# Performance work log

Hardware: AMD Instinct MI355X
Metric: run time of the kernel (lower is better)

The kernel has to match this reference:

```python
import jax, jax.numpy as jnp
import numpy as np

N, E, DIM, HEADS, EDGE_DIM = 50000, 800000, 128, 4, 1
C = DIM // HEADS  # per-head channels
EPS = 1e-5


def graph_ln(h, w, b):
    # PyG LayerNorm, mode='graph', batch=None: normalize over ALL nodes+features
    mu = h.mean()
    hc = h - mu
    std = jnp.sqrt(jnp.mean(hc * hc))
    return hc / (std + EPS) * w + b


def setup_inputs() -> dict:
    key = jax.random.key(0)
    ks = jax.random.split(key, 16)
    s = 1.0 / np.sqrt(DIM)
    return {
        "x": jax.random.normal(ks[0], (N, DIM), jnp.float32),
        "edge_index": jax.random.randint(ks[1], (2, E), 0, N, jnp.int32),
        "edge_weight": jax.random.uniform(ks[2], (E,), jnp.float32),
        "edge_attr": jax.random.normal(ks[3], (E, EDGE_DIM), jnp.float32),
        # GCNConv params
        "W_gcn": jax.random.normal(ks[4], (DIM, DIM), jnp.float32) * s,
        "b_gcn": jnp.zeros((DIM,), jnp.float32),
        # GATv2Conv params (share_weights=True -> single lin)
        "W_l": jax.random.normal(ks[5], (DIM, DIM), jnp.float32) * s,
        "b_l": jnp.zeros((DIM,), jnp.float32),
        "W_edge": jax.random.normal(ks[6], (EDGE_DIM, DIM), jnp.float32),
        "att": jax.random.normal(ks[7], (HEADS, C), jnp.float32) * (1.0 / np.sqrt(C)),
        "b_gat": jnp.zeros((DIM,), jnp.float32),
        # norms
        "gcn_nw": jnp.ones((DIM,), jnp.float32), "gcn_nb": jnp.zeros((DIM,), jnp.float32),
        "gat_nw": jnp.ones((DIM,), jnp.float32), "gat_nb": jnp.zeros((DIM,), jnp.float32),
        "out_nw": jnp.ones((DIM,), jnp.float32), "out_nb": jnp.zeros((DIM,), jnp.float32),
        "alpha": jnp.ones((2,), jnp.float32),
    }


def reference(x, edge_index, edge_weight, edge_attr, W_gcn, b_gcn, W_l, b_l,
              W_edge, att, b_gat, gcn_nw, gcn_nb, gat_nw, gat_nb, out_nw, out_nb, alpha):
    src, dst = edge_index[0], edge_index[1]

    # ---- GCN branch (normalize=True, add_self_loops=False) ----
    deg = jax.ops.segment_sum(edge_weight, dst, num_segments=N)
    dis = jnp.where(deg > 0, jax.lax.rsqrt(jnp.maximum(deg, 1e-30)), 0.0)
    norm = dis[src] * edge_weight * dis[dst]  # [E]
    xw = x @ W_gcn  # [N, DIM]
    h = jax.ops.segment_sum(norm[:, None] * xw[src], dst, num_segments=N) + b_gcn
    gcn_out = x + jax.nn.gelu(graph_ln(h, gcn_nw, gcn_nb), approximate=False)

    # ---- GATv2 branch (share_weights=True, edge_dim=1) ----
    xl = (x @ W_l + b_l).reshape(N, HEADS, C)
    e = (edge_attr @ W_edge).reshape(E, HEADS, C)
    z = jax.nn.leaky_relu(xl[dst] + xl[src] + e, negative_slope=0.2)  # [E,H,C]
    logits = jnp.einsum('ehc,hc->eh', z, att)  # [E,H]
    m = jax.ops.segment_max(logits, dst, num_segments=N)  # [N,H]
    a = jnp.exp(logits - m[dst])
    denom = jax.ops.segment_sum(a, dst, num_segments=N)
    a = a / (denom[dst] + 1e-16)  # softmax over incoming edges per dst, per head
    msg = xl[src] * a[:, :, None]  # [E,H,C]
    g = jax.ops.segment_sum(msg, dst, num_segments=N).reshape(N, DIM) + b_gat
    gat_out = x + jax.nn.gelu(graph_ln(g, gat_nw, gat_nb), approximate=False)

    # ---- fuse ----
    w = jax.nn.softmax(alpha)
    fused = w[0] * gcn_out + w[1] * gat_out
    return jax.nn.gelu(graph_ln(fused, out_nw, out_nb), approximate=False)
```

## Files before the change

kernel.cpp:

```cpp
#include <hip/hip_runtime.h>
#include <math.h>

#define DIM 128
#define HEADS 4
#define EPS 1e-5f
#define NBLK 1024

__device__ __forceinline__ float us2f(unsigned short u) {
  union { unsigned int i; float f; } c; c.i = ((unsigned int)u) << 16; return c.f;
}
__device__ __forceinline__ unsigned short f2us(float f) {
  union { float ff; unsigned int i; } c; c.ff = f;
  return (unsigned short)((c.i + 0x7FFFu + ((c.i >> 16) & 1u)) >> 16);
}
__device__ __forceinline__ float ldf(const void* p, size_t i, int fl32) {
  return fl32 ? ((const float*)p)[i] : us2f(((const unsigned short*)p)[i]);
}
__device__ __forceinline__ float gelu_exact(float v) {
  return 0.5f * v * (1.0f + erff(v * 0.7071067811865475f));
}

__global__ void __launch_bounds__(256)
k_detect(const unsigned short* __restrict__ x, long n, int* __restrict__ dflag) {
  long lim = n < 8192 ? n : 8192;
  int bad = 0;
  for (long i = threadIdx.x; i < lim; i += 256) {
    float v = us2f(x[i]);
    float a = fabsf(v);
    if (!(a == 0.0f || (a > 1e-30f && a < 1e3f))) bad++;
  }
  __shared__ int sb[256];
  sb[threadIdx.x] = bad;
  __syncthreads();
  for (int off = 128; off > 0; off >>= 1) {
    if ((int)threadIdx.x < off) sb[threadIdx.x] += sb[threadIdx.x + off];
    __syncthreads();
  }
  if (threadIdx.x == 0) dflag[0] = (sb[0] > 32) ? 1 : 0;
}

__global__ void k_deg_cnt(const int* __restrict__ dst, const void* __restrict__ ew,
                          float* __restrict__ deg, int* __restrict__ cnt, int E,
                          const int* __restrict__ df) {
  const int fl32 = *df;
  int e = blockIdx.x * blockDim.x + threadIdx.x;
  if (e < E) {
    int d = dst[e];
    float w = ldf(ew, e, fl32);
    if (isfinite(w)) atomicAdd(&deg[d], w);
    atomicAdd(&cnt[d], 1);
  }
}

__global__ void k_dis(float* __restrict__ deg, int N) {
  int i = blockIdx.x * blockDim.x + threadIdx.x;
  if (i < N) {
    float d = deg[i];
    deg[i] = (d > 0.0f) ? rsqrtf(fmaxf(d, 1e-30f)) : 0.0f;
  }
}

__global__ void __launch_bounds__(256)
k_scan(const int* __restrict__ cnt, int* __restrict__ off, int N, int E) {
  __shared__ int part[256];
  int t = threadIdx.x;
  int chunk = (N + 255) / 256;
  int lo = t * chunk;
  int hi = lo + chunk; if (hi > N) hi = N;
  int s = 0;
  for (int i = lo; i < hi; ++i) s += cnt[i];
  part[t] = s;
  __syncthreads();
  if (t == 0) {
    int run = 0;
    for (int j = 0; j < 256; ++j) { int tmp = part[j]; part[j] = run; run += tmp; }
  }
  __syncthreads();
  int run = part[t];
  for (int i = lo; i < hi; ++i) { off[i] = run; run += cnt[i]; }
  if (t == 0) off[N] = E;
}

__global__ void k_scatter(const int* __restrict__ src, const int* __restrict__ dst,
                          const void* __restrict__ ew, const void* __restrict__ ea,
                          const float* __restrict__ dis, const int* __restrict__ off,
                          int* __restrict__ cursor, int* __restrict__ csr_src,
                          float* __restrict__ csr_nm, float* __restrict__ csr_ea,
                          int E, const int* __restrict__ df) {
  const int fl32 = *df;
  int e = blockIdx.x * blockDim.x + threadIdx.x;
  if (e >= E) return;
  int d = dst[e], s = src[e];
  int pos = off[d] + atomicAdd(&cursor[d], 1);
  csr_src[pos] = s;
  float nm = dis[s] * ldf(ew, e, fl32) * dis[d];
  if (!isfinite(nm)) nm = 0.0f;
  csr_nm[pos] = nm;
  float eav = ldf(ea, e, fl32);
  if (!isfinite(eav)) eav = 0.0f;
  csr_ea[pos] = eav;
}

__global__ void __launch_bounds__(128)
k_gemm_dual(const void* __restrict__ x, const void* __restrict__ Wg,
            const void* __restrict__ Wl, const void* __restrict__ bl,
            unsigned short* __restrict__ xw, unsigned short* __restrict__ xl, int N,
            const int* __restrict__ df) {
  const int fl32 = *df;
  const int R = 8;
  __shared__ float xs[R][DIM];
  int c = threadIdx.x;
  int r0 = blockIdx.x * R;
  for (int r = 0; r < R; ++r) {
    int row = r0 + r;
    xs[r][c] = (row < N) ? ldf(x, (size_t)row * DIM + c, fl32) : 0.0f;
  }
  __syncthreads();
  float accg[R], accl[R];
  float blc = ldf(bl, c, fl32);
  #pragma unroll
  for (int r = 0; r < R; ++r) { accg[r] = 0.0f; accl[r] = blc; }
  for (int k = 0; k < DIM; ++k) {
    float wg = ldf(Wg, k * DIM + c, fl32);
    float wl = ldf(Wl, k * DIM + c, fl32);
    #pragma unroll
    for (int r = 0; r < R; ++r) {
      accg[r] = fmaf(xs[r][k], wg, accg[r]);
      accl[r] = fmaf(xs[r][k], wl, accl[r]);
    }
  }
  for (int r = 0; r < R; ++r) {
    int row = r0 + r;
    if (row < N) {
      float ag = accg[r], al = accl[r];
      if (!isfinite(ag)) ag = 0.0f;
      if (!isfinite(al)) al = 0.0f;
      xw[(size_t)row * DIM + c] = f2us(ag);
      xl[(size_t)row * DIM + c] = f2us(al);
    }
  }
}

__global__ void __launch_bounds__(256)
k_mega(const int* __restrict__ off, const int* __restrict__ csr_src,
       const float* __restrict__ csr_nm, const float* __restrict__ csr_ea,
       const unsigned short* __restrict__ xw, const unsigned short* __restrict__ xl,
       const void* __restrict__ Wed, const void* __restrict__ att,
       const void* __restrict__ bgcn, const void* __restrict__ bgat,
       float* __restrict__ h, float* __restrict__ g,
       double* __restrict__ pA, double* __restrict__ pB, int N,
       const int* __restrict__ df) {
  const int fl32 = *df;
  int wid = threadIdx.x >> 6;
  int lane = threadIdx.x & 63;
  int node = blockIdx.x * 4 + wid;
  int c0 = lane * 2;
  float wd0 = ldf(Wed, c0, fl32), wd1 = ldf(Wed, c0 + 1, fl32);
  float at0 = ldf(att, c0, fl32), at1 = ldf(att, c0 + 1, fl32);
  double sA = 0.0, sA2 = 0.0, sB = 0.0, sB2 = 0.0;
  if (node < N) {
    int beg = off[node], end = off[node + 1];
    float xd0 = us2f(xl[(size_t)node * DIM + c0]);
    float xd1 = us2f(xl[(size_t)node * DIM + c0 + 1]);
    float mx = -INFINITY, den = 0.f;
    float ga0 = 0.f, ga1 = 0.f, hc0 = 0.f, hc1 = 0.f;
    float eaP = 0.f, nmP = 0.f;
    ushort2 vP = make_ushort2(0, 0), uP = make_ushort2(0, 0);
    if (beg < end) {
      int s0 = csr_src[beg];
      eaP = csr_ea[beg];
      nmP = csr_nm[beg];
      vP = *(const ushort2*)(xl + (size_t)s0 * DIM + c0);
      uP = *(const ushort2*)(xw + (size_t)s0 * DIM + c0);
    }
    for (int i = beg; i < end; ++i) {
      float eav = eaP, nm = nmP;
      ushort2 v = vP, u = uP;
      int inext = i + 1;
      if (inext < end) {
        int sN = csr_src[inext];
        eaP = csr_ea[inext];
        nmP = csr_nm[inext];
        vP = *(const ushort2*)(xl + (size_t)sN * DIM + c0);
        uP = *(const ushort2*)(xw + (size_t)sN * DIM + c0);
      }
      float vx = us2f(v.x), vy = us2f(v.y);
      float z0 = xd0 + vx + eav * wd0; z0 = (z0 > 0.f) ? z0 : 0.2f * z0;
      float z1 = xd1 + vy + eav * wd1; z1 = (z1 > 0.f) ? z1 : 0.2f * z1;
      float dot = z0 * at0 + z1 * at1;
      dot += __shfl_xor(dot, 1);
      dot += __shfl_xor(dot, 2);
      dot += __shfl_xor(dot, 4);
      dot += __shfl_xor(dot, 8);
      if (!isfinite(dot)) dot = 0.0f;
      float nmx = fmaxf(mx, dot);
      float corr = __expf(mx - nmx);
      float w = __expf(dot - nmx);
      mx = nmx;
      den = fmaf(den, corr, w);
      ga0 = fmaf(ga0, corr, w * vx);
      ga1 = fmaf(ga1, corr, w * vy);
      hc0 = fmaf(nm, us2f(u.x), hc0);
      hc1 = fmaf(nm, us2f(u.y), hc1);
    }
    float inv = (end > beg) ? 1.0f / (den + 1e-16f) : 0.0f;
    ga0 *= inv; ga1 *= inv;
    if (!isfinite(ga0)) ga0 = 0.0f;
    if (!isfinite(ga1)) ga1 = 0.0f;
    if (!isfinite(hc0)) hc0 = 0.0f;
    if (!isfinite(hc1)) hc1 = 0.0f;
    *(float2*)(h + (size_t)node * DIM + c0) = make_float2(hc0, hc1);
    *(float2*)(g + (size_t)node * DIM + c0) = make_float2(ga0, ga1);
    float hA0 = hc0 + ldf(bgcn, c0, fl32), hA1 = hc1 + ldf(bgcn, c0 + 1, fl32);
    float gB0 = ga0 + ldf(bgat, c0, fl32), gB1 = ga1 + ldf(bgat, c0 + 1, fl32);
    sA  = (double)hA0 + (double)hA1;
    sA2 = (double)hA0 * hA0 + (double)hA1 * hA1;
    sB  = (double)gB0 + (double)gB1;
    sB2 = (double)gB0 * gB0 + (double)gB1 * gB1;
  }
  __shared__ double l1[256], l2[256], l3[256], l4[256];
  l1[threadIdx.x] = sA; l2[threadIdx.x] = sA2; l3[threadIdx.x] = sB; l4[threadIdx.x] = sB2;
  __syncthreads();
  for (int o = 128; o > 0; o >>= 1) {
    if ((int)threadIdx.x < o) {
      l1[threadIdx.x] += l1[threadIdx.x + o];
      l2[threadIdx.x] += l2[threadIdx.x + o];
      l3[threadIdx.x] += l3[threadIdx.x + o];
      l4[threadIdx.x] += l4[threadIdx.x + o];
    }
    __syncthreads();
  }
  if (threadIdx.x == 0) {
    pA[2 * blockIdx.x] = l1[0]; pA[2 * blockIdx.x + 1] = l2[0];
    pB[2 * blockIdx.x] = l3[0]; pB[2 * blockIdx.x + 1] = l4[0];
  }
}

__device__ __forceinline__ void ln_params(double S, double S2, double M, float* mu_out, float* sc_out) {
  double mu = S / M;
  double v = S2 / M - mu * mu;
  if (!(v > 0.0)) v = 0.0;
  float fmu = (float)mu;
  float sc = 1.0f / ((float)sqrt(v) + EPS);
  if (!isfinite(fmu)) fmu = 0.0f;
  if (!isfinite(sc)) sc = 0.0f;
  *mu_out = fmu; *sc_out = sc;
}

__global__ void __launch_bounds__(256)
k_fin12(const double* __restrict__ pA, const double* __restrict__ pB, int nblk,
        const void* __restrict__ alpha, float* __restrict__ params, double M,
        const int* __restrict__ df) {
  const int fl32 = *df;
  __shared__ double l1[256], l2[256], l3[256], l4[256];
  double a = 0, b = 0, c = 0, d = 0;
  for (int j = threadIdx.x; j < nblk; j += 256) {
    a += pA[2 * j]; b += pA[2 * j + 1];
    c += pB[2 * j]; d += pB[2 * j + 1];
  }
  l1[threadIdx.x] = a; l2[threadIdx.x] = b; l3[threadIdx.x] = c; l4[threadIdx.x] = d;
  __syncthreads();
  for (int off = 128; off > 0; off >>= 1) {
    if ((int)threadIdx.x < off) {
      l1[threadIdx.x] += l1[threadIdx.x + off];
      l2[threadIdx.x] += l2[threadIdx.x + off];
      l3[threadIdx.x] += l3[threadIdx.x + off];
      l4[threadIdx.x] += l4[threadIdx.x + off];
    }
    __syncthreads();
  }
  if (threadIdx.x == 0) {
    ln_params(l1[0], l2[0], M, &params[0], &params[1]);
    ln_params(l3[0], l4[0], M, &params[2], &params[3]);
    float a0 = ldf(alpha, 0, fl32), a1 = ldf(alpha, 1, fl32);
    if (!isfinite(a0)) a0 = 0.0f;
    if (!isfinite(a1)) a1 = 0.0f;
    float mx = fmaxf(a0, a1);
    float e0 = expf(a0 - mx), e1 = expf(a1 - mx);
    float inv = 1.0f / (e0 + e1);
    params[4] = e0 * inv;
    params[5] = e1 * inv;
  }
}

__global__ void __launch_bounds__(256)
k_fin3(const double* __restrict__ pC, float* __restrict__ params, double M) {
  __shared__ double l1[256], l2[256];
  double a = 0, b = 0;
  for (int j = threadIdx.x; j < NBLK; j += 256) { a += pC[2 * j]; b += pC[2 * j + 1]; }
  l1[threadIdx.x] = a; l2[threadIdx.x] = b;
  __syncthreads();
  for (int off = 128; off > 0; off >>= 1) {
    if ((int)threadIdx.x < off) {
      l1[threadIdx.x] += l1[threadIdx.x + off];
      l2[threadIdx.x] += l2[threadIdx.x + off];
    }
    __syncthreads();
  }
  if (threadIdx.x == 0) ln_params(l1[0], l2[0], M, &params[6], &params[7]);
}

__global__ void __launch_bounds__(256)
k_fuse(const void* __restrict__ x, float* h, const float* __restrict__ g,
       const void* __restrict__ b_gcn, const void* __restrict__ b_gat,
       const void* __restrict__ gcn_nw, const void* __restrict__ gcn_nb,
       const void* __restrict__ gat_nw, const void* __restrict__ gat_nb,
       const float* __restrict__ params, double* __restrict__ pC, long n,
       const int* __restrict__ df) {
  const int fl32 = *df;
  float mu1 = params[0], sc1 = params[1], mu2 = params[2], sc2 = params[3];
  float w0 = params[4], w1 = params[5];
  double s = 0.0, s2 = 0.0;
  long stride = (long)gridDim.x * blockDim.x;
  for (long i = (long)blockIdx.x * blockDim.x + threadIdx.x; i < n; i += stride) {
    size_t c = (size_t)(i & (DIM - 1));
    float xv = ldf(x, i, fl32);
    float hv = h[i] + ldf(b_gcn, c, fl32);
    float gv = g[i] + ldf(b_gat, c, fl32);
    float go = xv + gelu_exact((hv - mu1) * sc1 * ldf(gcn_nw, c, fl32) + ldf(gcn_nb, c, fl32));
    float ao = xv + gelu_exact((gv - mu2) * sc2 * ldf(gat_nw, c, fl32) + ldf(gat_nb, c, fl32));
    float f = w0 * go + w1 * ao;
    if (!isfinite(f)) f = 0.0f;
    h[i] = f;
    s += f; s2 += (double)f * f;
  }
  __shared__ double ls[256], ls2[256];
  ls[threadIdx.x] = s; ls2[threadIdx.x] = s2;
  __syncthreads();
  for (int off = 128; off > 0; off >>= 1) {
    if ((int)threadIdx.x < off) {
      ls[threadIdx.x] += ls[threadIdx.x + off];
      ls2[threadIdx.x] += ls2[threadIdx.x + off];
    }
    __syncthreads();
  }
  if (threadIdx.x == 0) { pC[2 * blockIdx.x] = ls[0]; pC[2 * blockIdx.x + 1] = ls2[0]; }
}

__global__ void k_final(const float* __restrict__ fused, const void* __restrict__ nw,
                        const void* __restrict__ nb, const float* __restrict__ params,
                        void* __restrict__ out, long n, const int* __restrict__ df) {
  const int fl32 = *df;
  long i = (long)blockIdx.x * blockDim.x + threadIdx.x;
  if (i >= n) return;
  size_t c = (size_t)(i & (DIM - 1));
  float mu = params[6], sc = params[7];
  float r = gelu_exact((fused[i] - mu) * sc * ldf(nw, c, fl32) + ldf(nb, c, fl32));
  if (!isfinite(r)) r = 0.0f;
  if (fl32) ((float*)out)[i] = r;
  else      ((unsigned short*)out)[i] = f2us(r);
}

extern "C" void kernel_launch(void* const* d_in, const int* in_sizes, int n_in,
                              void* d_out, int out_size, void* d_ws, size_t ws_size,
                              hipStream_t stream) {
  const void* x    = d_in[0];
  const int*  ei   = (const int*)d_in[1];
  const void* ew   = d_in[2];
  const void* ea   = d_in[3];
  const void* Wg   = d_in[4];
  const void* bgcn = d_in[5];
  const void* Wl   = d_in[6];
  const void* bl   = d_in[7];
  const void* Wed  = d_in[8];
  const void* att  = d_in[9];
  const void* bgat = d_in[10];
  const void* gcn_nw = d_in[11];
  const void* gcn_nb = d_in[12];
  const void* gat_nw = d_in[13];
  const void* gat_nb = d_in[14];
  const void* out_nw = d_in[15];
  const void* out_nb = d_in[16];
  const void* alpha  = d_in[17];

  const int N = in_sizes[0] / DIM;
  const int E = in_sizes[2];
  const int* src  = ei;
  const int* dstp = ei + E;
  const size_t ND = (size_t)N * DIM;
  const int nAgg = (N + 3) / 4;

  char* ws = (char*)d_ws;
  size_t o = 0;
  auto alloc = [&](size_t bytes) { size_t r = o; o += (bytes + 255) & ~(size_t)255; return r; };
  size_t o_deg    = alloc((size_t)N * 4);
  size_t o_cnt    = alloc((size_t)N * 4);
  size_t o_cursor = alloc((size_t)N * 4);
  size_t zero_end = o;
  size_t o_off    = alloc((size_t)(N + 1) * 4);
  size_t o_h      = alloc(ND * 4);
  size_t o_g      = alloc(ND * 4);
  size_t o_xw     = alloc(ND * 2);
  size_t o_xl     = alloc(ND * 2);
  size_t o_csrc   = alloc((size_t)E * 4);
  size_t o_cnm    = alloc((size_t)E * 4);
  size_t o_cea    = alloc((size_t)E * 4);
  size_t o_par    = alloc(8 * 4);
  size_t o_pA     = alloc((size_t)nAgg * 2 * 8);
  size_t o_pB     = alloc((size_t)nAgg * 2 * 8);
  size_t o_pC     = alloc((size_t)NBLK * 2 * 8);
  size_t o_flag   = alloc(4);
  (void)ws_size; (void)n_in; (void)out_size;

  float* deg     = (float*)(ws + o_deg);
  int*   cnt     = (int*)(ws + o_cnt);
  int*   cursor  = (int*)(ws + o_cursor);
  int*   off     = (int*)(ws + o_off);
  float* h       = (float*)(ws + o_h);
  float* g       = (float*)(ws + o_g);
  unsigned short* xw = (unsigned short*)(ws + o_xw);
  unsigned short* xl = (unsigned short*)(ws + o_xl);
  int*   csr_src = (int*)(ws + o_csrc);
  float* csr_nm  = (float*)(ws + o_cnm);
  float* csr_ea  = (float*)(ws + o_cea);
  float* params  = (float*)(ws + o_par);
  double* pA     = (double*)(ws + o_pA);
  double* pB     = (double*)(ws + o_pB);
  double* pC     = (double*)(ws + o_pC);
  int* dflag     = (int*)(ws + o_flag);

  hipMemsetAsync(ws, 0, zero_end, stream);
  k_detect<<<1, 256, 0, stream>>>((const unsigned short*)x, (long)ND, dflag);

  int ebk = (E + 255) / 256;
  k_deg_cnt<<<ebk, 256, 0, stream>>>(dstp, ew, deg, cnt, E, dflag);
  k_dis<<<(N + 255) / 256, 256, 0, stream>>>(deg, N);
  k_scan<<<1, 256, 0, stream>>>(cnt, off, N, E);
  k_scatter<<<ebk, 256, 0, stream>>>(src, dstp, ew, ea, deg, off, cursor,
                                     csr_src, csr_nm, csr_ea, E, dflag);

  k_gemm_dual<<<(N + 7) / 8, 128, 0, stream>>>(x, Wg, Wl, bl, xw, xl, N, dflag);

  k_mega<<<nAgg, 256, 0, stream>>>(off, csr_src, csr_nm, csr_ea, xw, xl,
                                   Wed, att, bgcn, bgat, h, g, pA, pB, N, dflag);

  k_fin12<<<1, 256, 0, stream>>>(pA, pB, nAgg, alpha, params, (double)ND, dflag);
  k_fuse<<<NBLK, 256, 0, stream>>>(x, h, g, bgcn, bgat, gcn_nw, gcn_nb, gat_nw, gat_nb,
                                   params, pC, (long)ND, dflag);
  k_fin3<<<1, 256, 0, stream>>>(pC, params, (double)ND);
  k_final<<<(int)((ND + 255) / 256), 256, 0, stream>>>(h, out_nw, out_nb, params,
                                                       d_out, (long)ND, dflag);
}
```

Measured before the change: 572.4 us.

## Use bf16 MFMA for dual GEMM, interleave xl/xw and pack CSR into int4

Replaces the scalar FMA dual GEMM with bf16 MFMA 16x16x32 using pre-swizzled weight fragments. The GEMM writes xl and xw interleaved per row, so the aggregation kernel fetches both with a single 8-byte gather per edge. CSR src/norm/edge_attr are packed into one int4 per edge, and the per-edge atomic rank is computed in the degree pass, which removes the cursor atomics from the scatter. The online softmax update is also rewritten to need one exp instead of two. The extra prepW kernel adds a launch, and the fp32 fallback path is a slow naive loop.

```diff
diff --git a/kernel.cpp b/kernel.cpp
--- a/kernel.cpp
+++ b/kernel.cpp
@@ -6,6 +6,10 @@
 #define EPS 1e-5f
 #define NBLK 1024
 
+typedef short frag_ab __attribute__((ext_vector_type(8)));
+typedef float f32x4 __attribute__((ext_vector_type(4)));
+typedef unsigned short us8 __attribute__((ext_vector_type(8)));
+
 __device__ __forceinline__ float us2f(unsigned short u) {
   union { unsigned int i; float f; } c; c.i = ((unsigned int)u) << 16; return c.f;
 }
@@ -19,6 +23,8 @@
 __device__ __forceinline__ float gelu_exact(float v) {
   return 0.5f * v * (1.0f + erff(v * 0.7071067811865475f));
 }
+
+__device__ __forceinline__ int packed_pos(int c) { return ((c & ~1) << 1) | (c & 1); }
 
 __global__ void __launch_bounds__(256)
 k_detect(const unsigned short* __restrict__ x, long n, int* __restrict__ dflag) {
@@ -40,15 +46,15 @@
 }
 
 __global__ void k_deg_cnt(const int* __restrict__ dst, const void* __restrict__ ew,
-                          float* __restrict__ deg, int* __restrict__ cnt, int E,
-                          const int* __restrict__ df) {
+                          float* __restrict__ deg, int* __restrict__ cnt,
+                          int* __restrict__ rank, int E, const int* __restrict__ df) {
   const int fl32 = *df;
   int e = blockIdx.x * blockDim.x + threadIdx.x;
   if (e < E) {
     int d = dst[e];
+    rank[e] = atomicAdd(&cnt[d], 1);
     float w = ldf(ew, e, fl32);
     if (isfinite(w)) atomicAdd(&deg[d], w);
-    atomicAdd(&cnt[d], 1);
   }
 }
 
@@ -84,67 +90,117 @@
 __global__ void k_scatter(const int* __restrict__ src, const int* __restrict__ dst,
                           const void* __restrict__ ew, const void* __restrict__ ea,
                           const float* __restrict__ dis, const int* __restrict__ off,
-                          int* __restrict__ cursor, int* __restrict__ csr_src,
-                          float* __restrict__ csr_nm, float* __restrict__ csr_ea,
+                          const int* __restrict__ rank, int4* __restrict__ csr,
                           int E, const int* __restrict__ df) {
   const int fl32 = *df;
   int e = blockIdx.x * blockDim.x + threadIdx.x;
   if (e >= E) return;
   int d = dst[e], s = src[e];
-  int pos = off[d] + atomicAdd(&cursor[d], 1);
-  csr_src[pos] = s;
+  int pos = off[d] + rank[e];
   float nm = dis[s] * ldf(ew, e, fl32) * dis[d];
   if (!isfinite(nm)) nm = 0.0f;
-  csr_nm[pos] = nm;
   float eav = ldf(ea, e, fl32);
   if (!isfinite(eav)) eav = 0.0f;
-  csr_ea[pos] = eav;
-}
-
-__global__ void __launch_bounds__(128)
-k_gemm_dual(const void* __restrict__ x, const void* __restrict__ Wg,
-            const void* __restrict__ Wl, const void* __restrict__ bl,
-            unsigned short* __restrict__ xw, unsigned short* __restrict__ xl, int N,
-            const int* __restrict__ df) {
-  const int fl32 = *df;
-  const int R = 8;
-  __shared__ float xs[R][DIM];
-  int c = threadIdx.x;
-  int r0 = blockIdx.x * R;
-  for (int r = 0; r < R; ++r) {
-    int row = r0 + r;
-    xs[r][c] = (row < N) ? ldf(x, (size_t)row * DIM + c, fl32) : 0.0f;
-  }
-  __syncthreads();
-  float accg[R], accl[R];
-  float blc = ldf(bl, c, fl32);
+  csr[pos] = make_int4(s, __float_as_int(nm), __float_as_int(eav), 0);
+}
+
+__global__ void __launch_bounds__(256)
+k_prepW(const unsigned short* __restrict__ Wg, const unsigned short* __restrict__ Wl,
+        unsigned short* __restrict__ Wtg, unsigned short* __restrict__ Wtl) {
+  int idx = blockIdx.x * 256 + threadIdx.x;
+  if (idx >= 2048) return;
+  int kc = idx >> 9, rem = idx & 511, nt = rem >> 6, lane = rem & 63;
+  int quad = lane >> 4, n = lane & 15;
   #pragma unroll
-  for (int r = 0; r < R; ++r) { accg[r] = 0.0f; accl[r] = blc; }
-  for (int k = 0; k < DIM; ++k) {
-    float wg = ldf(Wg, k * DIM + c, fl32);
-    float wl = ldf(Wl, k * DIM + c, fl32);
+  for (int j = 0; j < 8; ++j) {
+    int srcIdx = (kc * 32 + quad * 8 + j) * DIM + nt * 16 + n;
+    Wtg[idx * 8 + j] = Wg[srcIdx];
+    Wtl[idx * 8 + j] = Wl[srcIdx];
+  }
+}
+
+__global__ void __launch_bounds__(256)
+k_gemm(const void* __restrict__ x, const void* __restrict__ Wg, const void* __restrict__ Wl,
+       const void* __restrict__ bl, const unsigned short* __restrict__ Wtg,
+       const unsigned short* __restrict__ Wtl, unsigned short* __restrict__ packed,
+       int N, const int* __restrict__ df) {
+  const int fl32 = *df;
+  __shared__ unsigned short tiles[4][16][256];
+  int wid = threadIdx.x >> 6, lane = threadIdx.x & 63;
+  int quad = lane >> 4, m = lane & 15;
+  int row0 = blockIdx.x * 64 + wid * 16;
+  if (!fl32) {
+    const unsigned short* xb = (const unsigned short*)x;
+    int rowm = row0 + m;
+    frag_ab a[4];
     #pragma unroll
-    for (int r = 0; r < R; ++r) {
-      accg[r] = fmaf(xs[r][k], wg, accg[r]);
-      accl[r] = fmaf(xs[r][k], wl, accl[r]);
-    }
-  }
-  for (int r = 0; r < R; ++r) {
-    int row = r0 + r;
-    if (row < N) {
-      float ag = accg[r], al = accl[r];
-      if (!isfinite(ag)) ag = 0.0f;
-      if (!isfinite(al)) al = 0.0f;
-      xw[(size_t)row * DIM + c] = f2us(ag);
-      xl[(size_t)row * DIM + c] = f2us(al);
-    }
-  }
-}
-
-__global__ void __launch_bounds__(256)
-k_mega(const int* __restrict__ off, const int* __restrict__ csr_src,
-       const float* __restrict__ csr_nm, const float* __restrict__ csr_ea,
-       const unsigned short* __restrict__ xw, const unsigned short* __restrict__ xl,
+    for (int kc = 0; kc < 4; ++kc) {
+      if (rowm < N) a[kc] = *(const frag_ab*)(xb + (size_t)rowm * DIM + kc * 32 + quad * 8);
+      else { frag_ab z; for (int j = 0; j < 8; ++j) z[j] = 0; a[kc] = z; }
+    }
+    f32x4 accG[8], accL[8];
+    #pragma unroll
+    for (int nt = 0; nt < 8; ++nt)
+      for (int r = 0; r < 4; ++r) { accG[nt][r] = 0.f; accL[nt][r] = 0.f; }
+    #pragma unroll
+    for (int nt = 0; nt < 8; ++nt) {
+      #pragma unroll
+      for (int kc = 0; kc < 4; ++kc) {
+        frag_ab bg = *(const frag_ab*)(Wtg + ((size_t)(kc * 8 + nt) * 64 + lane) * 8);
+        frag_ab bf = *(const frag_ab*)(Wtl + ((size_t)(kc * 8 + nt) * 64 + lane) * 8);
+        accG[nt] = __builtin_amdgcn_mfma_f32_16x16x32_bf16(a[kc], bg, accG[nt], 0, 0, 0);
+        accL[nt] = __builtin_amdgcn_mfma_f32_16x16x32_bf16(a[kc], bf, accL[nt], 0, 0, 0);
+      }
+    }
+    #pragma unroll
+    for (int nt = 0; nt < 8; ++nt) {
+      int c = nt * 16 + m;
+      float blc = us2f(((const unsigned short*)bl)[c]);
+      int pos = packed_pos(c);
+      #pragma unroll
+      for (int r = 0; r < 4; ++r) {
+        int row = quad * 4 + r;
+        float vG = accG[nt][r];
+        float vL = accL[nt][r] + blc;
+        if (!isfinite(vG)) vG = 0.f;
+        if (!isfinite(vL)) vL = 0.f;
+        tiles[wid][row][pos] = f2us(vL);
+        tiles[wid][row][pos + 2] = f2us(vG);
+      }
+    }
+    __syncthreads();
+    #pragma unroll
+    for (int t = 0; t < 8; ++t) {
+      int flat = t * 512 + lane * 8;
+      int r = flat >> 8, cp = flat & 255;
+      int grow = row0 + r;
+      if (grow < N)
+        *(us8*)(packed + (size_t)grow * 256 + cp) = *(const us8*)&tiles[wid][r][cp];
+    }
+  } else {
+    int c = threadIdx.x & 127;
+    float blc = ldf(bl, c, 1);
+    for (int rr = (threadIdx.x >> 7); rr < 64; rr += 2) {
+      int row = blockIdx.x * 64 + rr;
+      if (row >= N) continue;
+      float ag = 0.f, al = blc;
+      for (int k = 0; k < DIM; ++k) {
+        float xv = ldf(x, (size_t)row * DIM + k, 1);
+        ag = fmaf(xv, ldf(Wg, k * DIM + c, 1), ag);
+        al = fmaf(xv, ldf(Wl, k * DIM + c, 1), al);
+      }
+      if (!isfinite(ag)) ag = 0.f;
+      if (!isfinite(al)) al = 0.f;
+      int pos = packed_pos(c);
+      packed[(size_t)row * 256 + pos] = f2us(al);
+      packed[(size_t)row * 256 + pos + 2] = f2us(ag);
+    }
+  }
+}
+
+__global__ void __launch_bounds__(256)
+k_mega(const int* __restrict__ off, const int4* __restrict__ csr,
+       const unsigned short* __restrict__ packed,
        const void* __restrict__ Wed, const void* __restrict__ att,
        const void* __restrict__ bgcn, const void* __restrict__ bgat,
        float* __restrict__ h, float* __restrict__ g,
@@ -160,30 +216,23 @@
   double sA = 0.0, sA2 = 0.0, sB = 0.0, sB2 = 0.0;
   if (node < N) {
     int beg = off[node], end = off[node + 1];
-    float xd0 = us2f(xl[(size_t)node * DIM + c0]);
-    float xd1 = us2f(xl[(size_t)node * DIM + c0 + 1]);
+    ushort4 xd = *(const ushort4*)(packed + (size_t)node * 256 + lane * 4);
+    float xd0 = us2f(xd.x), xd1 = us2f(xd.y);
     float mx = -INFINITY, den = 0.f;
     float ga0 = 0.f, ga1 = 0.f, hc0 = 0.f, hc1 = 0.f;
-    float eaP = 0.f, nmP = 0.f;
-    ushort2 vP = make_ushort2(0, 0), uP = make_ushort2(0, 0);
+    int4 cP = make_int4(0, 0, 0, 0);
+    ushort4 vP = make_ushort4(0, 0, 0, 0);
     if (beg < end) {
-      int s0 = csr_src[beg];
-      eaP = csr_ea[beg];
-      nmP = csr_nm[beg];
-      vP = *(const ushort2*)(xl + (size_t)s0 * DIM + c0);
-      uP = *(const ushort2*)(xw + (size_t)s0 * DIM + c0);
+      cP = csr[beg];
+      vP = *(const ushort4*)(packed + (size_t)cP.x * 256 + lane * 4);
     }
     for (int i = beg; i < end; ++i) {
-      float eav = eaP, nm = nmP;
-      ushort2 v = vP, u = uP;
-      int inext = i + 1;
-      if (inext < end) {
-        int sN = csr_src[inext];
-        eaP = csr_ea[inext];
-        nmP = csr_nm[inext];
-        vP = *(const ushort2*)(xl + (size_t)sN * DIM + c0);
-        uP = *(const ushort2*)(xw + (size_t)sN * DIM + c0);
+      int4 ce = cP; ushort4 v = vP;
+      if (i + 1 < end) {
+        cP = csr[i + 1];
+        vP = *(const ushort4*)(packed + (size_t)cP.x * 256 + lane * 4);
       }
+      float nm = __int_as_float(ce.y), eav = __int_as_float(ce.z);
       float vx = us2f(v.x), vy = us2f(v.y);
       float z0 = xd0 + vx + eav * wd0; z0 = (z0 > 0.f) ? z0 : 0.2f * z0;
       float z1 = xd1 + vy + eav * wd1; z1 = (z1 > 0.f) ? z1 : 0.2f * z1;
@@ -192,16 +241,16 @@
       dot += __shfl_xor(dot, 2);
       dot += __shfl_xor(dot, 4);
       dot += __shfl_xor(dot, 8);
-      if (!isfinite(dot)) dot = 0.0f;
-      float nmx = fmaxf(mx, dot);
-      float corr = __expf(mx - nmx);
-      float w = __expf(dot - nmx);
-      mx = nmx;
+      float e = __expf(-fabsf(dot - mx));
+      bool up = dot > mx;
+      float corr = up ? e : 1.0f;
+      float w = up ? 1.0f : e;
+      mx = up ? dot : mx;
       den = fmaf(den, corr, w);
       ga0 = fmaf(ga0, corr, w * vx);
       ga1 = fmaf(ga1, corr, w * vy);
-      hc0 = fmaf(nm, us2f(u.x), hc0);
-      hc1 = fmaf(nm, us2f(u.y), hc1);
+      hc0 = fmaf(nm, us2f(v.z), hc0);
+      hc1 = fmaf(nm, us2f(v.w), hc1);
     }
     float inv = (end > beg) ? 1.0f / (den + 1e-16f) : 0.0f;
     ga0 *= inv; ga1 *= inv;
@@ -385,16 +434,14 @@
   auto alloc = [&](size_t bytes) { size_t r = o; o += (bytes + 255) & ~(size_t)255; return r; };
   size_t o_deg    = alloc((size_t)N * 4);
   size_t o_cnt    = alloc((size_t)N * 4);
-  size_t o_cursor = alloc((size_t)N * 4);
   size_t zero_end = o;
   size_t o_off    = alloc((size_t)(N + 1) * 4);
   size_t o_h      = alloc(ND * 4);
   size_t o_g      = alloc(ND * 4);
-  size_t o_xw     = alloc(ND * 2);
-  size_t o_xl     = alloc(ND * 2);
-  size_t o_csrc   = alloc((size_t)E * 4);
-  size_t o_cnm    = alloc((size_t)E * 4);
-  size_t o_cea    = alloc((size_t)E * 4);
+  size_t o_packed = alloc(ND * 4);
+  size_t o_csr    = alloc((size_t)E * 16);
+  size_t o_wtg    = alloc(2048 * 8 * 2);
+  size_t o_wtl    = alloc(2048 * 8 * 2);
   size_t o_par    = alloc(8 * 4);
   size_t o_pA     = alloc((size_t)nAgg * 2 * 8);
   size_t o_pB     = alloc((size_t)nAgg * 2 * 8);
@@ -404,15 +451,14 @@
 
   float* deg     = (float*)(ws + o_deg);
   int*   cnt     = (int*)(ws + o_cnt);
-  int*   cursor  = (int*)(ws + o_cursor);
   int*   off     = (int*)(ws + o_off);
   float* h       = (float*)(ws + o_h);
+  int*   rank    = (int*)(ws + o_h);
   float* g       = (float*)(ws + o_g);
-  unsigned short* xw = (unsigned short*)(ws + o_xw);
-  unsigned short* xl = (unsigned short*)(ws + o_xl);
-  int*   csr_src = (int*)(ws + o_csrc);
-  float* csr_nm  = (float*)(ws + o_cnm);
-  float* csr_ea  = (float*)(ws + o_cea);
+  unsigned short* packed = (unsigned short*)(ws + o_packed);
+  int4*  csr     = (int4*)(ws + o_csr);
+  unsigned short* Wtg = (unsigned short*)(ws + o_wtg);
+  unsigned short* Wtl = (unsigned short*)(ws + o_wtl);
   float* params  = (float*)(ws + o_par);
   double* pA     = (double*)(ws + o_pA);
   double* pB     = (double*)(ws + o_pB);
@@ -423,16 +469,16 @@
   k_detect<<<1, 256, 0, stream>>>((const unsigned short*)x, (long)ND, dflag);
 
   int ebk = (E + 255) / 256;
-  k_deg_cnt<<<ebk, 256, 0, stream>>>(dstp, ew, deg, cnt, E, dflag);
+  k_deg_cnt<<<ebk, 256, 0, stream>>>(dstp, ew, deg, cnt, rank, E, dflag);
   k_dis<<<(N + 255) / 256, 256, 0, stream>>>(deg, N);
   k_scan<<<1, 256, 0, stream>>>(cnt, off, N, E);
-  k_scatter<<<ebk, 256, 0, stream>>>(src, dstp, ew, ea, deg, off, cursor,
-                                     csr_src, csr_nm, csr_ea, E, dflag);
-
-  k_gemm_dual<<<(N + 7) / 8, 128, 0, stream>>>(x, Wg, Wl, bl, xw, xl, N, dflag);
-
-  k_mega<<<nAgg, 256, 0, stream>>>(off, csr_src, csr_nm, csr_ea, xw, xl,
-                                   Wed, att, bgcn, bgat, h, g, pA, pB, N, dflag);
+  k_scatter<<<ebk, 256, 0, stream>>>(src, dstp, ew, ea, deg, off, rank, csr, E, dflag);
+
+  k_prepW<<<8, 256, 0, stream>>>((const unsigned short*)Wg, (const unsigned short*)Wl, Wtg, Wtl);
+  k_gemm<<<(N + 63) / 64, 256, 0, stream>>>(x, Wg, Wl, bl, Wtg, Wtl, packed, N, dflag);
+
+  k_mega<<<nAgg, 256, 0, stream>>>(off, csr, packed, Wed, att, bgcn, bgat,
+                                   h, g, pA, pB, N, dflag);
 
   k_fin12<<<1, 256, 0, stream>>>(pA, pB, nAgg, alpha, params, (double)ND, dflag);
   k_fuse<<<NBLK, 256, 0, stream>>>(x, h, g, bgcn, bgat, gcn_nw, gcn_nb, gat_nw, gat_nb,
```

New measurement: 851.7 us. 1.49x slower.

## Interleave xl/xw rows and pack CSR edge data into int4 records

Applied to the files above, without the earlier changes.

The GEMM now writes xl and xw interleaved per node, so each lane fetches its two xl and two xw values with one 8-byte gather instead of two separate loads. CSR src, norm and edge attribute are packed into one 16-byte record, so each edge needs one load. The scatter reuses a per-edge rank taken from the degree-count atomics instead of a second atomic cursor pass, and the online softmax uses one exp per edge instead of two. The costs are a padded CSR array, rank stored in the h buffer, and dropping the non-finite guard on the logit.

```diff
diff --git a/kernel.cpp b/kernel.cpp
--- a/kernel.cpp
+++ b/kernel.cpp
@@ -19,6 +19,8 @@
 __device__ __forceinline__ float gelu_exact(float v) {
   return 0.5f * v * (1.0f + erff(v * 0.7071067811865475f));
 }
+
+__device__ __forceinline__ int packed_pos(int c) { return ((c & ~1) << 1) | (c & 1); }
 
 __global__ void __launch_bounds__(256)
 k_detect(const unsigned short* __restrict__ x, long n, int* __restrict__ dflag) {
@@ -40,15 +42,15 @@
 }
 
 __global__ void k_deg_cnt(const int* __restrict__ dst, const void* __restrict__ ew,
-                          float* __restrict__ deg, int* __restrict__ cnt, int E,
-                          const int* __restrict__ df) {
+                          float* __restrict__ deg, int* __restrict__ cnt,
+                          int* __restrict__ rank, int E, const int* __restrict__ df) {
   const int fl32 = *df;
   int e = blockIdx.x * blockDim.x + threadIdx.x;
   if (e < E) {
     int d = dst[e];
+    rank[e] = atomicAdd(&cnt[d], 1);
     float w = ldf(ew, e, fl32);
     if (isfinite(w)) atomicAdd(&deg[d], w);
-    atomicAdd(&cnt[d], 1);
   }
 }
 
@@ -84,28 +86,24 @@
 __global__ void k_scatter(const int* __restrict__ src, const int* __restrict__ dst,
                           const void* __restrict__ ew, const void* __restrict__ ea,
                           const float* __restrict__ dis, const int* __restrict__ off,
-                          int* __restrict__ cursor, int* __restrict__ csr_src,
-                          float* __restrict__ csr_nm, float* __restrict__ csr_ea,
+                          const int* __restrict__ rank, int4* __restrict__ csr,
                           int E, const int* __restrict__ df) {
   const int fl32 = *df;
   int e = blockIdx.x * blockDim.x + threadIdx.x;
   if (e >= E) return;
   int d = dst[e], s = src[e];
-  int pos = off[d] + atomicAdd(&cursor[d], 1);
-  csr_src[pos] = s;
+  int pos = off[d] + rank[e];
   float nm = dis[s] * ldf(ew, e, fl32) * dis[d];
   if (!isfinite(nm)) nm = 0.0f;
-  csr_nm[pos] = nm;
   float eav = ldf(ea, e, fl32);
   if (!isfinite(eav)) eav = 0.0f;
-  csr_ea[pos] = eav;
+  csr[pos] = make_int4(s, __float_as_int(nm), __float_as_int(eav), 0);
 }
 
 __global__ void __launch_bounds__(128)
-k_gemm_dual(const void* __restrict__ x, const void* __restrict__ Wg,
-            const void* __restrict__ Wl, const void* __restrict__ bl,
-            unsigned short* __restrict__ xw, unsigned short* __restrict__ xl, int N,
-            const int* __restrict__ df) {
+k_gemm(const void* __restrict__ x, const void* __restrict__ Wg,
+       const void* __restrict__ Wl, const void* __restrict__ bl,
+       unsigned short* __restrict__ packed, int N, const int* __restrict__ df) {
   const int fl32 = *df;
   const int R = 8;
   __shared__ float xs[R][DIM];
@@ -129,22 +127,22 @@
       accl[r] = fmaf(xs[r][k], wl, accl[r]);
     }
   }
+  int pos = packed_pos(c);
   for (int r = 0; r < R; ++r) {
     int row = r0 + r;
     if (row < N) {
       float ag = accg[r], al = accl[r];
       if (!isfinite(ag)) ag = 0.0f;
       if (!isfinite(al)) al = 0.0f;
-      xw[(size_t)row * DIM + c] = f2us(ag);
-      xl[(size_t)row * DIM + c] = f2us(al);
-    }
-  }
-}
-
-__global__ void __launch_bounds__(256)
-k_mega(const int* __restrict__ off, const int* __restrict__ csr_src,
-       const float* __restrict__ csr_nm, const float* __restrict__ csr_ea,
-       const unsigned short* __restrict__ xw, const unsigned short* __restrict__ xl,
+      packed[(size_t)row * 256 + pos] = f2us(al);
+      packed[(size_t)row * 256 + pos + 2] = f2us(ag);
+    }
+  }
+}
+
+__global__ void __launch_bounds__(256)
+k_mega(const int* __restrict__ off, const int4* __restrict__ csr,
+       const unsigned short* __restrict__ packed,
        const void* __restrict__ Wed, const void* __restrict__ att,
        const void* __restrict__ bgcn, const void* __restrict__ bgat,
        float* __restrict__ h, float* __restrict__ g,
@@ -160,30 +158,23 @@
   double sA = 0.0, sA2 = 0.0, sB = 0.0, sB2 = 0.0;
   if (node < N) {
     int beg = off[node], end = off[node + 1];
-    float xd0 = us2f(xl[(size_t)node * DIM + c0]);
-    float xd1 = us2f(xl[(size_t)node * DIM + c0 + 1]);
+    ushort4 xd = *(const ushort4*)(packed + (size_t)node * 256 + lane * 4);
+    float xd0 = us2f(xd.x), xd1 = us2f(xd.y);
     float mx = -INFINITY, den = 0.f;
     float ga0 = 0.f, ga1 = 0.f, hc0 = 0.f, hc1 = 0.f;
-    float eaP = 0.f, nmP = 0.f;
-    ushort2 vP = make_ushort2(0, 0), uP = make_ushort2(0, 0);
+    int4 cP = make_int4(0, 0, 0, 0);
+    ushort4 vP = make_ushort4(0, 0, 0, 0);
     if (beg < end) {
-      int s0 = csr_src[beg];
-      eaP = csr_ea[beg];
-      nmP = csr_nm[beg];
-      vP = *(const ushort2*)(xl + (size_t)s0 * DIM + c0);
-      uP = *(const ushort2*)(xw + (size_t)s0 * DIM + c0);
+      cP = csr[beg];
+      vP = *(const ushort4*)(packed + (size_t)cP.x * 256 + lane * 4);
     }
     for (int i = beg; i < end; ++i) {
-      float eav = eaP, nm = nmP;
-      ushort2 v = vP, u = uP;
-      int inext = i + 1;
-      if (inext < end) {
-        int sN = csr_src[inext];
-        eaP = csr_ea[inext];
-        nmP = csr_nm[inext];
-        vP = *(const ushort2*)(xl + (size_t)sN * DIM + c0);
-        uP = *(const ushort2*)(xw + (size_t)sN * DIM + c0);
+      int4 ce = cP; ushort4 v = vP;
+      if (i + 1 < end) {
+        cP = csr[i + 1];
+        vP = *(const ushort4*)(packed + (size_t)cP.x * 256 + lane * 4);
       }
+      float nm = __int_as_float(ce.y), eav = __int_as_float(ce.z);
       float vx = us2f(v.x), vy = us2f(v.y);
       float z0 = xd0 + vx + eav * wd0; z0 = (z0 > 0.f) ? z0 : 0.2f * z0;
       float z1 = xd1 + vy + eav * wd1; z1 = (z1 > 0.f) ? z1 : 0.2f * z1;
@@ -192,16 +183,16 @@
       dot += __shfl_xor(dot, 2);
       dot += __shfl_xor(dot, 4);
       dot += __shfl_xor(dot, 8);
-      if (!isfinite(dot)) dot = 0.0f;
-      float nmx = fmaxf(mx, dot);
-      float corr = __expf(mx - nmx);
-      float w = __expf(dot - nmx);
-      mx = nmx;
+      float e = __expf(-fabsf(dot - mx));
+      bool up = dot > mx;
+      float corr = up ? e : 1.0f;
+      float w = up ? 1.0f : e;
+      mx = up ? dot : mx;
       den = fmaf(den, corr, w);
       ga0 = fmaf(ga0, corr, w * vx);
       ga1 = fmaf(ga1, corr, w * vy);
-      hc0 = fmaf(nm, us2f(u.x), hc0);
-      hc1 = fmaf(nm, us2f(u.y), hc1);
+      hc0 = fmaf(nm, us2f(v.z), hc0);
+      hc1 = fmaf(nm, us2f(v.w), hc1);
     }
     float inv = (end > beg) ? 1.0f / (den + 1e-16f) : 0.0f;
     ga0 *= inv; ga1 *= inv;
@@ -385,16 +376,12 @@
   auto alloc = [&](size_t bytes) { size_t r = o; o += (bytes + 255) & ~(size_t)255; return r; };
   size_t o_deg    = alloc((size_t)N * 4);
   size_t o_cnt    = alloc((size_t)N * 4);
-  size_t o_cursor = alloc((size_t)N * 4);
   size_t zero_end = o;
   size_t o_off    = alloc((size_t)(N + 1) * 4);
   size_t o_h      = alloc(ND * 4);
   size_t o_g      = alloc(ND * 4);
-  size_t o_xw     = alloc(ND * 2);
-  size_t o_xl     = alloc(ND * 2);
-  size_t o_csrc   = alloc((size_t)E * 4);
-  size_t o_cnm    = alloc((size_t)E * 4);
-  size_t o_cea    = alloc((size_t)E * 4);
+  size_t o_packed = alloc(ND * 4);
+  size_t o_csr    = alloc((size_t)E * 16);
   size_t o_par    = alloc(8 * 4);
   size_t o_pA     = alloc((size_t)nAgg * 2 * 8);
   size_t o_pB     = alloc((size_t)nAgg * 2 * 8);
@@ -404,15 +391,12 @@
 
   float* deg     = (float*)(ws + o_deg);
   int*   cnt     = (int*)(ws + o_cnt);
-  int*   cursor  = (int*)(ws + o_cursor);
   int*   off     = (int*)(ws + o_off);
   float* h       = (float*)(ws + o_h);
+  int*   rank    = (int*)(ws + o_h);
   float* g       = (float*)(ws + o_g);
-  unsigned short* xw = (unsigned short*)(ws + o_xw);
-  unsigned short* xl = (unsigned short*)(ws + o_xl);
-  int*   csr_src = (int*)(ws + o_csrc);
-  float* csr_nm  = (float*)(ws + o_cnm);
-  float* csr_ea  = (float*)(ws + o_cea);
+  unsigned short* packed = (unsigned short*)(ws + o_packed);
+  int4*  csr     = (int4*)(ws + o_csr);
   float* params  = (float*)(ws + o_par);
   double* pA     = (double*)(ws + o_pA);
   double* pB     = (double*)(ws + o_pB);
@@ -423,16 +407,15 @@
   k_detect<<<1, 256, 0, stream>>>((const unsigned short*)x, (long)ND, dflag);
 
   int ebk = (E + 255) / 256;
-  k_deg_cnt<<<ebk, 256, 0, stream>>>(dstp, ew, deg, cnt, E, dflag);
+  k_deg_cnt<<<ebk, 256, 0, stream>>>(dstp, ew, deg, cnt, rank, E, dflag);
   k_dis<<<(N + 255) / 256, 256, 0, stream>>>(deg, N);
   k_scan<<<1, 256, 0, stream>>>(cnt, off, N, E);
-  k_scatter<<<ebk, 256, 0, stream>>>(src, dstp, ew, ea, deg, off, cursor,
-                                     csr_src, csr_nm, csr_ea, E, dflag);
-
-  k_gemm_dual<<<(N + 7) / 8, 128, 0, stream>>>(x, Wg, Wl, bl, xw, xl, N, dflag);
-
-  k_mega<<<nAgg, 256, 0, stream>>>(off, csr_src, csr_nm, csr_ea, xw, xl,
-                                   Wed, att, bgcn, bgat, h, g, pA, pB, N, dflag);
+  k_scatter<<<ebk, 256, 0, stream>>>(src, dstp, ew, ea, deg, off, rank, csr, E, dflag);
+
+  k_gemm<<<(N + 7) / 8, 128, 0, stream>>>(x, Wg, Wl, bl, packed, N, dflag);
+
+  k_mega<<<nAgg, 256, 0, stream>>>(off, csr, packed, Wed, att, bgcn, bgat,
+                                   h, g, pA, pB, N, dflag);
 
   k_fin12<<<1, 256, 0, stream>>>(pA, pB, nAgg, alpha, params, (double)ND, dflag);
   k_fuse<<<NBLK, 256, 0, stream>>>(x, h, g, bgcn, bgat, gcn_nw, gcn_nb, gat_nw, gat_nb,
```

After: 560.4 us. 2.1% less time.
